# Performance work log

Measured on AMD Instinct MI355X. Metric: run time of the kernel, lower is better.

Reference implementation:

```python
import jax, jax.numpy as jnp
import numpy as np

VOCAB, EMBED, NFEAT, T, HIDDEN, NCLASS, BATCH = 50000, 50, 3, 120, 300, 5, 1024
D_IN = NFEAT * EMBED  # 150


def setup_inputs() -> dict:
    key = jax.random.key(0)
    ks = jax.random.split(key, 5)
    s_in = 1.0 / np.sqrt(D_IN)
    s_h = 1.0 / np.sqrt(HIDDEN)
    return {
        "ids": jax.random.randint(ks[0], (BATCH, T, NFEAT), 0, VOCAB, dtype=jnp.int32),
        "embed": jax.random.normal(ks[1], (VOCAB, EMBED), dtype=jnp.float32),
        "Wx": jax.random.normal(ks[2], (D_IN, 4 * HIDDEN), dtype=jnp.float32) * s_in,
        "Wh": jax.random.normal(ks[3], (HIDDEN, 4 * HIDDEN), dtype=jnp.float32) * s_h,
        "b": jnp.zeros((4 * HIDDEN,), dtype=jnp.float32),
        "U": jax.random.normal(ks[4], (HIDDEN, NCLASS), dtype=jnp.float32) * s_h,
        "b2": jnp.zeros((NCLASS,), dtype=jnp.float32),
    }


def reference(ids, embed, Wx, Wh, b, U, b2):
    # Embedding lookup + concat windows: (B, T, 3) -> (B, T, 150)
    x = embed[ids].reshape(ids.shape[0], T, D_IN)
    # Precompute input contribution for all timesteps: (B, T, 4H)
    xz = jnp.einsum("btd,dg->btg", x, Wx) + b
    xz = jnp.transpose(xz, (1, 0, 2))  # (T, B, 4H)

    def step(carry, xz_t):
        c, h = carry
        z = xz_t + h @ Wh  # (B, 4H)
        i, f, g, o = jnp.split(z, 4, axis=-1)
        i = jax.nn.sigmoid(i)
        f = jax.nn.sigmoid(f)
        o = jax.nn.sigmoid(o)
        g = jnp.tanh(g)
        c = f * c + i * g
        h = o * jnp.tanh(c)
        # dropout at inference (keep_prob=1) is identity
        y = h @ U + b2  # (B, C)
        return (c, h), y

    B = ids.shape[0]
    init = (jnp.zeros((B, HIDDEN), x.dtype), jnp.zeros((B, HIDDEN), x.dtype))
    _, ys = jax.lax.scan(step, init, xz)  # ys: (T, B, C)
    return jnp.transpose(ys, (1, 0, 2))  # (B, T, C)
```

## Files before the change

### kernel.cpp

```cpp
#include <hip/hip_runtime.h>


#define BATCH 1024
#define TT    120
#define HID   300
#define KX    160
#define KH    320
#define SL    64
#define HSL   60
#define NCOL  1280
#define GH    5
#define GB    32
#define BS    32
#define XST   168
#define FSTR  32
#define NSLOT 3
#define NB    256
#define NREL  (GH * 4)

typedef __attribute__((ext_vector_type(8))) short bf16x8;
typedef __attribute__((ext_vector_type(4))) float f32x4;

__device__ __forceinline__ unsigned short f2b(float f) {
  union { float f; unsigned u; } v; v.f = f;
  unsigned r = v.u + 0x7fffu + ((v.u >> 16) & 1u);
  return (unsigned short)(r >> 16);
}
__device__ __forceinline__ float sigm(float x) {
  return __builtin_amdgcn_rcpf(1.f + __expf(-x));
}
__device__ __forceinline__ float tanhf_(float x) {
  return 2.f * __builtin_amdgcn_rcpf(1.f + __expf(-2.f * x)) - 1.f;
}
__device__ __forceinline__ void mfma_bA(bf16x8 a, const bf16x8& b, f32x4& c) {
  asm("v_mfma_f32_16x16x32_bf16 %0, %1, %2, %0" : "+v"(c) : "v"(a), "a"(b));
}

__global__ void k_reorder_wh(const float* __restrict__ W, unsigned short* __restrict__ Wp) {
  int tid = blockIdx.x * 256 + threadIdx.x;
  if (tid >= KH * NCOL) return;
  int c = tid % NCOL, k = tid / NCOL;
  int js = k >> 6, v0 = k & 63;
  int j = c >> 8, r = c & 255, g = r >> 6, u0 = r & 63;
  float val = 0.f;
  if (v0 < HSL && u0 < HSL) val = W[(js * HSL + v0) * 1200 + g * 300 + j * HSL + u0];
  Wp[((k >> 3) * NCOL + c) * 8 + (k & 7)] = f2b(val);
}

__global__ void k_reorder_wx(const float* __restrict__ W, unsigned short* __restrict__ Wp) {
  int tid = blockIdx.x * 256 + threadIdx.x;
  if (tid >= KX * NCOL) return;
  int c = tid % NCOL, k = tid / NCOL;
  int j = c >> 8, r = c & 255, g = r >> 6, u0 = r & 63;
  float val = 0.f;
  if (k < 150 && u0 < HSL) val = W[k * 1200 + g * 300 + j * HSL + u0];
  Wp[((k >> 3) * NCOL + c) * 8 + (k & 7)] = f2b(val);
}

__global__ void k_reorder_b(const float* __restrict__ b, float* __restrict__ bp) {
  int c = blockIdx.x * 256 + threadIdx.x;
  if (c >= NCOL) return;
  int j = c >> 8, r = c & 255, g = r >> 6, u0 = r & 63;
  bp[c] = (u0 < HSL) ? b[g * 300 + j * HSL + u0] : 0.f;
}

__global__ void k_reorder_u(const float* __restrict__ U, unsigned short* __restrict__ Up) {
  int tid = blockIdx.x * 256 + threadIdx.x;
  if (tid >= KH * 16) return;
  int n = tid % 16, k = tid / 16;
  int js = k >> 6, v0 = k & 63;
  float v = (v0 < HSL && n < 5) ? U[(js * HSL + v0) * 5 + n] : 0.f;
  Up[((k >> 3) * 16 + n) * 8 + (k & 7)] = f2b(v);
}

__global__ void k_init(int* __restrict__ flags, int n, int* __restrict__ xcd_cnt) {
  int i = blockIdx.x * 256 + threadIdx.x;
  if (i < n)
    __hip_atomic_store(flags + i, 0, __ATOMIC_RELAXED, __HIP_MEMORY_SCOPE_AGENT);
  if (i < 8)
    __hip_atomic_store(xcd_cnt + i, 0, __ATOMIC_RELAXED, __HIP_MEMORY_SCOPE_AGENT);
}

__launch_bounds__(256, 1)
__global__ void k_lstm(const int* __restrict__ ids, const float* __restrict__ embed,
                       const unsigned short* __restrict__ Wp,
                       const unsigned short* __restrict__ Wxp,
                       const float* __restrict__ bp,
                       const unsigned short* __restrict__ Up,
                       unsigned short* __restrict__ hbuf,
                       int* __restrict__ flags,
                       int* __restrict__ xcd_cnt,
                       const float* __restrict__ b2,
                       float* __restrict__ out) {
  __shared__ __align__(16) unsigned short x_lds[2][BS * XST];
  __shared__ char lds_pad[61440];
  __shared__ int role[2];

  const int tid = threadIdx.x;
  if (tid == 0) {
    ((volatile char*)lds_pad)[0] = 0;
    int xcd = __builtin_amdgcn_s_getreg(63508) & 7;
    int rank = atomicAdd(&xcd_cnt[xcd], 1);
    role[0] = xcd; role[1] = rank;
  }
  __syncthreads();
  const int xcd = role[0], rank = role[1];
  if (rank >= GH * 4) return;
  const int bg = xcd * 4 + rank / GH;
  const int j  = rank % GH;

  const int lane = tid & 63, w = tid >> 6;
  const int l15 = lane & 15, l4 = lane >> 4;

  if (tid < BS) {
#pragma unroll
    for (int bq = 0; bq < 2; ++bq)
      for (int e = 150; e < XST; ++e) x_lds[bq][tid * XST + e] = 0;
  }

  const int colb = j * 256 + w * 16 + l15;

  bf16x8 bh[10][4], bx[5][4];
#pragma unroll
  for (int kk = 0; kk < 10; ++kk)
#pragma unroll
    for (int g = 0; g < 4; ++g)
      bh[kk][g] = *(const bf16x8*)(Wp + ((kk * 4 + l4) * NCOL + colb + g * 64) * 8);
#pragma unroll
  for (int kk = 0; kk < 5; ++kk)
#pragma unroll
    for (int g = 0; g < 4; ++g)
      bx[kk][g] = *(const bf16x8*)(Wxp + ((kk * 4 + l4) * NCOL + colb + g * 64) * 8);

  float bias[4];
#pragma unroll
  for (int g = 0; g < 4; ++g) bias[g] = bp[colb + g * 64];
  const float b2v = (l15 < 5) ? b2[l15] : 0.f;

  int xrow = 0, koff = 0, nf2 = 0, f = 0;
  const bool gth = (tid < 192);
  if (gth) {
    xrow = tid / 6; int half = tid % 6; f = half >> 1; int hh = half & 1;
    nf2 = hh ? 12 : 13;
    koff = f * 50 + (hh ? 26 : 0);
  }
  const long idbase = (long)(bg * BS + xrow) * TT * 3 + f;
  const int  eoff   = (koff - f * 50);

  if (gth) {
    int id0 = ids[idbase + 0 * 3];
    const float* src = embed + (long)id0 * 50 + eoff;
    unsigned short* dst = &x_lds[0][xrow * XST + koff];
#pragma unroll
    for (int e = 0; e < 13; ++e)
      if (e < nf2) {
        float2 v = *(const float2*)(src + 2 * e);
        *(unsigned*)(dst + 2 * e) = (unsigned)f2b(v.x) | ((unsigned)f2b(v.y) << 16);
      }
  }
  __syncthreads();

  f32x4 acc[4][2];
  float cst[2][4];
#pragma unroll
  for (int g = 0; g < 4; ++g)
#pragma unroll
    for (int mt = 0; mt < 2; ++mt) acc[g][mt] = {0.f, 0.f, 0.f, 0.f};
#pragma unroll
  for (int mt = 0; mt < 2; ++mt)
#pragma unroll
    for (int r = 0; r < 4; ++r) cst[mt][r] = 0.f;

  {
    const unsigned short* xb = &x_lds[0][l15 * XST + l4 * 8];
#pragma unroll
    for (int kk = 0; kk < 5; ++kk) {
      bf16x8 a0 = *(const bf16x8*)(xb + kk * 32);
      bf16x8 a1 = *(const bf16x8*)(xb + 16 * XST + kk * 32);
#pragma unroll
      for (int g = 0; g < 4; ++g) {
        mfma_bA(a0, bx[kk][g], acc[g][0]);
        mfma_bA(a1, bx[kk][g], acc[g][1]);
      }
    }
  }

  float2 xv[13];
  int idv = 0;
  if (gth) {
    int id1 = ids[idbase + 1 * 3];
    const float* src = embed + (long)id1 * 50 + eoff;
#pragma unroll
    for (int e = 0; e < 13; ++e)
      if (e < nf2) xv[e] = *(const float2*)(src + 2 * e);
    idv = ids[idbase + 2 * 3];
  }

  bf16x8 va0[10], va1[10];

  for (int t = 0; t < TT; ++t) {
    if (t > 0) {
      if (lane == 0) {
        const int* fp = flags + ((t - 1) * GB + bg) * FSTR;
        int it = 0;
        while (__hip_atomic_load(fp, __ATOMIC_RELAXED, __HIP_MEMORY_SCOPE_AGENT) < NREL) {
          if (++it > 500000) break;
        }
      }
      asm volatile("buffer_inv\n\ts_waitcnt vmcnt(0)" ::: "memory");

      const unsigned short* ar =
          hbuf + ((t - 1) % NSLOT) * (BATCH * KH) + (bg * BS + l15) * KH + l4 * 8;
#pragma unroll
      for (int kk = 0; kk < 10; ++kk) {
        va0[kk] = *(const bf16x8*)(ar + kk * 32);
        va1[kk] = *(const bf16x8*)(ar + 16 * KH + kk * 32);
      }
#pragma unroll
      for (int kk = 0; kk < 10; ++kk) {
#pragma unroll
        for (int g = 0; g < 4; ++g) {
          mfma_bA(va0[kk], bh[kk][g], acc[g][0]);
          mfma_bA(va1[kk], bh[kk][g], acc[g][1]);
        }
      }
    }

    unsigned short* hdst = hbuf + (t % NSLOT) * (BATCH * KH);
#pragma unroll
    for (int mt = 0; mt < 2; ++mt) {
#pragma unroll
      for (int r = 0; r < 4; ++r) {
        float zi = acc[0][mt][r] + bias[0];
        float zf = acc[1][mt][r] + bias[1];
        float zg = acc[2][mt][r] + bias[2];
        float zo = acc[3][mt][r] + bias[3];
        float gi = sigm(zi), gf = sigm(zf), go = sigm(zo), gg = tanhf_(zg);
        float c = gf * cst[mt][r] + gi * gg;
        cst[mt][r] = c;
        float h = go * tanhf_(c);
        unsigned v = f2b(h);
        unsigned p1 = v | ((unsigned)__shfl_xor((int)v, 1) << 16);
        unsigned long long p2 = (unsigned long long)p1 |
            ((unsigned long long)(unsigned)__shfl_xor((int)p1, 2) << 32);
        if ((l15 & 3) == 0) {
          int row = bg * BS + mt * 16 + l4 * 4 + r;
          *(unsigned long long*)(hdst + row * KH + j * SL + w * 16 + l15) = p2;
        }
      }
      acc[0][mt] = {0.f, 0.f, 0.f, 0.f};
      acc[1][mt] = {0.f, 0.f, 0.f, 0.f};
      acc[2][mt] = {0.f, 0.f, 0.f, 0.f};
      acc[3][mt] = {0.f, 0.f, 0.f, 0.f};
    }

    asm volatile("s_waitcnt vmcnt(0)" ::: "memory");
    if (lane == 0)
      __hip_atomic_fetch_add(flags + (t * GB + bg) * FSTR, 1, __ATOMIC_RELAXED,
                             __HIP_MEMORY_SCOPE_AGENT);

    if (t > 0 && j == (t - 1) % GH) {
      if (w == 2) {
        f32x4 ay = {0.f, 0.f, 0.f, 0.f};
#pragma unroll
        for (int kk = 0; kk < 10; ++kk) {
          bf16x8 u = *(const bf16x8*)(Up + ((kk * 4 + l4) * 16 + l15) * 8);
          ay = __builtin_amdgcn_mfma_f32_16x16x32_bf16(va0[kk], u, ay, 0, 0, 0);
        }
        if (l15 < 5)
#pragma unroll
          for (int q = 0; q < 4; ++q)
            out[((bg * BS + l4 * 4 + q) * TT + (t - 1)) * 5 + l15] = ay[q] + b2v;
      } else if (w == 3) {
        f32x4 ay = {0.f, 0.f, 0.f, 0.f};
#pragma unroll
        for (int kk = 0; kk < 10; ++kk) {
          bf16x8 u = *(const bf16x8*)(Up + ((kk * 4 + l4) * 16 + l15) * 8);
          ay = __builtin_amdgcn_mfma_f32_16x16x32_bf16(va1[kk], u, ay, 0, 0, 0);
        }
        if (l15 < 5)
#pragma unroll
          for (int q = 0; q < 4; ++q)
            out[((bg * BS + 16 + l4 * 4 + q) * TT + (t - 1)) * 5 + l15] = ay[q] + b2v;
      }
    }

    if (t + 1 < TT) {
      if (gth) {
        unsigned short* dst = &x_lds[(t + 1) & 1][xrow * XST + koff];
#pragma unroll
        for (int e = 0; e < 13; ++e)
          if (e < nf2)
            *(unsigned*)(dst + 2 * e) = (unsigned)f2b(xv[e].x) | ((unsigned)f2b(xv[e].y) << 16);
      }
      __syncthreads();
      const unsigned short* xb = &x_lds[(t + 1) & 1][l15 * XST + l4 * 8];
#pragma unroll
      for (int kk = 0; kk < 5; ++kk) {
        bf16x8 a0 = *(const bf16x8*)(xb + kk * 32);
        bf16x8 a1 = *(const bf16x8*)(xb + 16 * XST + kk * 32);
#pragma unroll
        for (int g = 0; g < 4; ++g) {
          mfma_bA(a0, bx[kk][g], acc[g][0]);
          mfma_bA(a1, bx[kk][g], acc[g][1]);
        }
      }
      if (gth && t + 2 < TT) {
        const float* src = embed + (long)idv * 50 + eoff;
#pragma unroll
        for (int e = 0; e < 13; ++e)
          if (e < nf2) xv[e] = *(const float2*)(src + 2 * e);
        if (t + 3 < TT) idv = ids[idbase + (long)(t + 3) * 3];
      }
    }
  }

  if (j == (TT - 1) % GH) {
    if (lane == 0) {
      const int* fp = flags + ((TT - 1) * GB + bg) * FSTR;
      int it = 0;
      while (__hip_atomic_load(fp, __ATOMIC_RELAXED, __HIP_MEMORY_SCOPE_AGENT) < NREL) {
        if (++it > 500000) break;
      }
    }
    asm volatile("buffer_inv\n\ts_waitcnt vmcnt(0)" ::: "memory");
    const unsigned short* ar =
        hbuf + ((TT - 1) % NSLOT) * (BATCH * KH) + (bg * BS + l15) * KH + l4 * 8;
#pragma unroll
    for (int kk = 0; kk < 10; ++kk) {
      va0[kk] = *(const bf16x8*)(ar + kk * 32);
      va1[kk] = *(const bf16x8*)(ar + 16 * KH + kk * 32);
    }
    if (w == 2) {
      f32x4 ay = {0.f, 0.f, 0.f, 0.f};
#pragma unroll
      for (int kk = 0; kk < 10; ++kk) {
        bf16x8 u = *(const bf16x8*)(Up + ((kk * 4 + l4) * 16 + l15) * 8);
        ay = __builtin_amdgcn_mfma_f32_16x16x32_bf16(va0[kk], u, ay, 0, 0, 0);
      }
      if (l15 < 5)
#pragma unroll
        for (int q = 0; q < 4; ++q)
          out[((bg * BS + l4 * 4 + q) * TT + (TT - 1)) * 5 + l15] = ay[q] + b2v;
    } else if (w == 3) {
      f32x4 ay = {0.f, 0.f, 0.f, 0.f};
#pragma unroll
      for (int kk = 0; kk < 10; ++kk) {
        bf16x8 u = *(const bf16x8*)(Up + ((kk * 4 + l4) * 16 + l15) * 8);
        ay = __builtin_amdgcn_mfma_f32_16x16x32_bf16(va1[kk], u, ay, 0, 0, 0);
      }
      if (l15 < 5)
#pragma unroll
        for (int q = 0; q < 4; ++q)
          out[((bg * BS + 16 + l4 * 4 + q) * TT + (TT - 1)) * 5 + l15] = ay[q] + b2v;
    }
  }
}

extern "C" void kernel_launch(void* const* d_in, const int* in_sizes, int n_in,
                              void* d_out, int out_size, void* d_ws, size_t ws_size,
                              hipStream_t stream) {
  const int*   ids   = (const int*)d_in[0];
  const float* embed = (const float*)d_in[1];
  const float* Wx    = (const float*)d_in[2];
  const float* Wh    = (const float*)d_in[3];
  const float* b     = (const float*)d_in[4];
  const float* U     = (const float*)d_in[5];
  const float* b2    = (const float*)d_in[6];
  float* out = (float*)d_out;

  char* ws = (char*)d_ws;
  size_t off = 0;
  unsigned short* Wp   = (unsigned short*)(ws + off); off += (size_t)KH * NCOL * 2;
  unsigned short* Wxp  = (unsigned short*)(ws + off); off += (size_t)KX * NCOL * 2;
  float*          bp   = (float*)(ws + off);          off += (size_t)NCOL * 4;
  unsigned short* Up   = (unsigned short*)(ws + off); off += (size_t)KH * 16 * 2;
  unsigned short* hbuf = (unsigned short*)(ws + off); off += (size_t)NSLOT * BATCH * KH * 2;
  int*            flags= (int*)(ws + off);            off += (size_t)TT * GB * FSTR * 4;
  int*            xcd_cnt = (int*)(ws + off);         off += 8 * 4;
  if (ws_size < off) return;

  k_init<<<(TT * GB * FSTR + 255) / 256, 256, 0, stream>>>(flags, TT * GB * FSTR, xcd_cnt);
  k_reorder_wh<<<(KH * NCOL + 255) / 256, 256, 0, stream>>>(Wh, Wp);
  k_reorder_wx<<<(KX * NCOL + 255) / 256, 256, 0, stream>>>(Wx, Wxp);
  k_reorder_b<<<(NCOL + 255) / 256, 256, 0, stream>>>(b, bp);
  k_reorder_u<<<(KH * 16 + 255) / 256, 256, 0, stream>>>(U, Up);

  k_lstm<<<dim3(NB), dim3(256), 0, stream>>>(ids, embed, Wp, Wxp, bp, Up,
                                             hbuf, flags, xcd_cnt, b2, out);
}
```

Measured before the change: 671.9 us.

## Offload output projection to dedicated blocks and replace atomic counters with per-wave flags

Adds four extra blocks per XCD whose only job is to compute the per-step output projection h@U, so the recurrent blocks no longer do it on the critical path. The atomic-add step counter becomes 20 per-wave flag words, each set to -1 with a plain store, and every wave polls and ANDs them. Flag clearing moves into the kernel behind a ready barrier, and the h ring buffer grows to 8 slots so the trailing projection blocks cannot be overwritten. The cost is more polling traffic, reliance on extra resident blocks, and bounded spin loops that could break early and break correctness.

```diff
diff --git a/kernel.cpp b/kernel.cpp
--- a/kernel.cpp
+++ b/kernel.cpp
@@ -14,9 +14,8 @@
 #define BS    32
 #define XST   168
 #define FSTR  32
-#define NSLOT 3
+#define NSLOT 8
 #define NB    256
-#define NREL  (GH * 4)
 
 typedef __attribute__((ext_vector_type(8))) short bf16x8;
 typedef __attribute__((ext_vector_type(4))) float f32x4;
@@ -34,6 +33,17 @@
 }
 __device__ __forceinline__ void mfma_bA(bf16x8 a, const bf16x8& b, f32x4& c) {
   asm("v_mfma_f32_16x16x32_bf16 %0, %1, %2, %0" : "+v"(c) : "v"(a), "a"(b));
+}
+__device__ __forceinline__ void poll20(const int* fl) {
+  int it = 0;
+  while (true) {
+    asm volatile("buffer_inv\n\ts_waitcnt vmcnt(0)" ::: "memory");
+    const volatile int* f = (const volatile int*)fl;
+    int a = f[0] & f[1] & f[2] & f[3] & f[4] & f[5] & f[6] & f[7] & f[8] & f[9] &
+            f[10] & f[11] & f[12] & f[13] & f[14] & f[15] & f[16] & f[17] & f[18] & f[19];
+    if (a == -1) break;
+    if (++it > 50000) break;
+  }
 }
 
 __global__ void k_reorder_wh(const float* __restrict__ W, unsigned short* __restrict__ Wp) {
@@ -73,10 +83,10 @@
   Up[((k >> 3) * 16 + n) * 8 + (k & 7)] = f2b(v);
 }
 
-__global__ void k_init(int* __restrict__ flags, int n, int* __restrict__ xcd_cnt) {
+__global__ void k_init(int* __restrict__ ready, int* __restrict__ xcd_cnt) {
   int i = blockIdx.x * 256 + threadIdx.x;
-  if (i < n)
-    __hip_atomic_store(flags + i, 0, __ATOMIC_RELAXED, __HIP_MEMORY_SCOPE_AGENT);
+  if (i < GB * FSTR)
+    __hip_atomic_store(ready + i, 0, __ATOMIC_RELAXED, __HIP_MEMORY_SCOPE_AGENT);
   if (i < 8)
     __hip_atomic_store(xcd_cnt + i, 0, __ATOMIC_RELAXED, __HIP_MEMORY_SCOPE_AGENT);
 }
@@ -89,6 +99,7 @@
                        const unsigned short* __restrict__ Up,
                        unsigned short* __restrict__ hbuf,
                        int* __restrict__ flags,
+                       int* __restrict__ ready,
                        int* __restrict__ xcd_cnt,
                        const float* __restrict__ b2,
                        float* __restrict__ out) {
@@ -105,12 +116,62 @@
   }
   __syncthreads();
   const int xcd = role[0], rank = role[1];
-  if (rank >= GH * 4) return;
-  const int bg = xcd * 4 + rank / GH;
-  const int j  = rank % GH;
+  if (rank >= GH * 4 + 4) return;
+  const bool is_y = (rank >= GH * 4);
+  const int bg = xcd * 4 + (is_y ? (rank - GH * 4) : rank / GH);
+  const int j  = is_y ? 0 : rank % GH;
 
   const int lane = tid & 63, w = tid >> 6;
   const int l15 = lane & 15, l4 = lane >> 4;
+  const float b2v = (l15 < 5) ? b2[l15] : 0.f;
+
+  if (is_y) {
+    if (w >= 2) return;
+    bf16x8 up[10];
+#pragma unroll
+    for (int kk = 0; kk < 10; ++kk)
+      up[kk] = *(const bf16x8*)(Up + ((kk * 4 + l4) * 16 + l15) * 8);
+    {
+      int it = 0;
+      while (__hip_atomic_load(ready + bg * FSTR, __ATOMIC_RELAXED,
+                               __HIP_MEMORY_SCOPE_AGENT) < GH) {
+        __builtin_amdgcn_s_sleep(2);
+        if (++it > 200000) break;
+      }
+    }
+    for (int t = 0; t < TT; ++t) {
+      poll20(flags + (t * GB + bg) * FSTR);
+      const unsigned short* ar =
+          hbuf + (t % NSLOT) * (BATCH * KH) + (bg * BS + w * 16 + l15) * KH + l4 * 8;
+      f32x4 ay = {0.f, 0.f, 0.f, 0.f};
+#pragma unroll
+      for (int kk = 0; kk < 10; ++kk) {
+        bf16x8 a = *(const bf16x8*)(ar + kk * 32);
+        ay = __builtin_amdgcn_mfma_f32_16x16x32_bf16(a, up[kk], ay, 0, 0, 0);
+      }
+      if (l15 < 5)
+#pragma unroll
+        for (int q = 0; q < 4; ++q)
+          out[((bg * BS + w * 16 + l4 * 4 + q) * TT + t) * 5 + l15] = ay[q] + b2v;
+    }
+    return;
+  }
+
+  {
+    for (int tt = lane; tt < TT; tt += 64)
+      ((volatile int*)(flags + (tt * GB + bg) * FSTR))[j * 4 + w] = 0;
+    asm volatile("s_waitcnt vmcnt(0)" ::: "memory");
+    __syncthreads();
+    if (tid == 0)
+      __hip_atomic_fetch_add(ready + bg * FSTR, 1, __ATOMIC_RELAXED,
+                             __HIP_MEMORY_SCOPE_AGENT);
+    int it = 0;
+    while (__hip_atomic_load(ready + bg * FSTR, __ATOMIC_RELAXED,
+                             __HIP_MEMORY_SCOPE_AGENT) < GH) {
+      __builtin_amdgcn_s_sleep(2);
+      if (++it > 200000) break;
+    }
+  }
 
   if (tid < BS) {
 #pragma unroll
@@ -135,7 +196,6 @@
   float bias[4];
 #pragma unroll
   for (int g = 0; g < 4; ++g) bias[g] = bp[colb + g * 64];
-  const float b2v = (l15 < 5) ? b2[l15] : 0.f;
 
   int xrow = 0, koff = 0, nf2 = 0, f = 0;
   const bool gth = (tid < 192);
@@ -200,14 +260,7 @@
 
   for (int t = 0; t < TT; ++t) {
     if (t > 0) {
-      if (lane == 0) {
-        const int* fp = flags + ((t - 1) * GB + bg) * FSTR;
-        int it = 0;
-        while (__hip_atomic_load(fp, __ATOMIC_RELAXED, __HIP_MEMORY_SCOPE_AGENT) < NREL) {
-          if (++it > 500000) break;
-        }
-      }
-      asm volatile("buffer_inv\n\ts_waitcnt vmcnt(0)" ::: "memory");
+      poll20(flags + ((t - 1) * GB + bg) * FSTR);
 
       const unsigned short* ar =
           hbuf + ((t - 1) % NSLOT) * (BATCH * KH) + (bg * BS + l15) * KH + l4 * 8;
@@ -256,34 +309,7 @@
 
     asm volatile("s_waitcnt vmcnt(0)" ::: "memory");
     if (lane == 0)
-      __hip_atomic_fetch_add(flags + (t * GB + bg) * FSTR, 1, __ATOMIC_RELAXED,
-                             __HIP_MEMORY_SCOPE_AGENT);
-
-    if (t > 0 && j == (t - 1) % GH) {
-      if (w == 2) {
-        f32x4 ay = {0.f, 0.f, 0.f, 0.f};
-#pragma unroll
-        for (int kk = 0; kk < 10; ++kk) {
-          bf16x8 u = *(const bf16x8*)(Up + ((kk * 4 + l4) * 16 + l15) * 8);
-          ay = __builtin_amdgcn_mfma_f32_16x16x32_bf16(va0[kk], u, ay, 0, 0, 0);
-        }
-        if (l15 < 5)
-#pragma unroll
-          for (int q = 0; q < 4; ++q)
-            out[((bg * BS + l4 * 4 + q) * TT + (t - 1)) * 5 + l15] = ay[q] + b2v;
-      } else if (w == 3) {
-        f32x4 ay = {0.f, 0.f, 0.f, 0.f};
-#pragma unroll
-        for (int kk = 0; kk < 10; ++kk) {
-          bf16x8 u = *(const bf16x8*)(Up + ((kk * 4 + l4) * 16 + l15) * 8);
-          ay = __builtin_amdgcn_mfma_f32_16x16x32_bf16(va1[kk], u, ay, 0, 0, 0);
-        }
-        if (l15 < 5)
-#pragma unroll
-          for (int q = 0; q < 4; ++q)
-            out[((bg * BS + 16 + l4 * 4 + q) * TT + (t - 1)) * 5 + l15] = ay[q] + b2v;
-      }
-    }
+      ((volatile int*)(flags + (t * GB + bg) * FSTR))[j * 4 + w] = -1;
 
     if (t + 1 < TT) {
       if (gth) {
@@ -312,47 +338,6 @@
           if (e < nf2) xv[e] = *(const float2*)(src + 2 * e);
         if (t + 3 < TT) idv = ids[idbase + (long)(t + 3) * 3];
       }
-    }
-  }
-
-  if (j == (TT - 1) % GH) {
-    if (lane == 0) {
-      const int* fp = flags + ((TT - 1) * GB + bg) * FSTR;
-      int it = 0;
-      while (__hip_atomic_load(fp, __ATOMIC_RELAXED, __HIP_MEMORY_SCOPE_AGENT) < NREL) {
-        if (++it > 500000) break;
-      }
-    }
-    asm volatile("buffer_inv\n\ts_waitcnt vmcnt(0)" ::: "memory");
-    const unsigned short* ar =
-        hbuf + ((TT - 1) % NSLOT) * (BATCH * KH) + (bg * BS + l15) * KH + l4 * 8;
-#pragma unroll
-    for (int kk = 0; kk < 10; ++kk) {
-      va0[kk] = *(const bf16x8*)(ar + kk * 32);
-      va1[kk] = *(const bf16x8*)(ar + 16 * KH + kk * 32);
-    }
-    if (w == 2) {
-      f32x4 ay = {0.f, 0.f, 0.f, 0.f};
-#pragma unroll
-      for (int kk = 0; kk < 10; ++kk) {
-        bf16x8 u = *(const bf16x8*)(Up + ((kk * 4 + l4) * 16 + l15) * 8);
-        ay = __builtin_amdgcn_mfma_f32_16x16x32_bf16(va0[kk], u, ay, 0, 0, 0);
-      }
-      if (l15 < 5)
-#pragma unroll
-        for (int q = 0; q < 4; ++q)
-          out[((bg * BS + l4 * 4 + q) * TT + (TT - 1)) * 5 + l15] = ay[q] + b2v;
-    } else if (w == 3) {
-      f32x4 ay = {0.f, 0.f, 0.f, 0.f};
-#pragma unroll
-      for (int kk = 0; kk < 10; ++kk) {
-        bf16x8 u = *(const bf16x8*)(Up + ((kk * 4 + l4) * 16 + l15) * 8);
-        ay = __builtin_amdgcn_mfma_f32_16x16x32_bf16(va1[kk], u, ay, 0, 0, 0);
-      }
-      if (l15 < 5)
-#pragma unroll
-        for (int q = 0; q < 4; ++q)
-          out[((bg * BS + 16 + l4 * 4 + q) * TT + (TT - 1)) * 5 + l15] = ay[q] + b2v;
     }
   }
 }
@@ -377,15 +362,16 @@
   unsigned short* Up   = (unsigned short*)(ws + off); off += (size_t)KH * 16 * 2;
   unsigned short* hbuf = (unsigned short*)(ws + off); off += (size_t)NSLOT * BATCH * KH * 2;
   int*            flags= (int*)(ws + off);            off += (size_t)TT * GB * FSTR * 4;
+  int*            ready= (int*)(ws + off);            off += (size_t)GB * FSTR * 4;
   int*            xcd_cnt = (int*)(ws + off);         off += 8 * 4;
   if (ws_size < off) return;
 
-  k_init<<<(TT * GB * FSTR + 255) / 256, 256, 0, stream>>>(flags, TT * GB * FSTR, xcd_cnt);
+  k_init<<<(GB * FSTR + 255) / 256, 256, 0, stream>>>(ready, xcd_cnt);
   k_reorder_wh<<<(KH * NCOL + 255) / 256, 256, 0, stream>>>(Wh, Wp);
   k_reorder_wx<<<(KX * NCOL + 255) / 256, 256, 0, stream>>>(Wx, Wxp);
   k_reorder_b<<<(NCOL + 255) / 256, 256, 0, stream>>>(b, bp);
   k_reorder_u<<<(KH * 16 + 255) / 256, 256, 0, stream>>>(U, Up);
 
   k_lstm<<<dim3(NB), dim3(256), 0, stream>>>(ids, embed, Wp, Wxp, bp, Up,
-                                             hbuf, flags, xcd_cnt, b2, out);
-}
+                                             hbuf, flags, ready, xcd_cnt, b2, out);
+}
```

Result: slower. 904.2 us (+34.6%).
